# Kernel tuning notes

Hardware: AMD Instinct MI355X
Metric: run time of the kernel (lower is better)

## Reference

```python
import jax, jax.numpy as jnp
import numpy as np

B, S, HID, NH, INTER, VOCAB = 8, 1024, 512, 8, 2048, 30522
EPS = 1e-12


def _layernorm(x, w, b):
    m = jnp.mean(x, axis=-1, keepdims=True)
    v = jnp.mean((x - m) ** 2, axis=-1, keepdims=True)
    return (x - m) * jax.lax.rsqrt(v + EPS) * w + b


def _multihead_mut(x, M):
    # x: (b, s, d); M: (H, s, s). Split d into H heads, mix along the
    # sequence axis per head: out[b,t,h,d] = sum_s x[b,s,h,d] * M[h,s,t]
    b, s, d = x.shape
    xh = x.reshape(b, s, NH, d // NH)
    out = jnp.einsum('bshd,hst->bthd', xh, M)
    return out.reshape(b, s, d)


def setup_inputs() -> dict:
    key = jax.random.key(0)
    ks = jax.random.split(key, 14)
    g = lambda i, shape, scale: jax.random.normal(ks[i], shape, dtype=jnp.float32) * scale
    return {
        'x': jax.random.randint(ks[0], (B, S), 0, VOCAB),
        'word_emb': g(1, (VOCAB, HID), 0.02),
        'pos_emb': g(2, (S, HID), 0.02),
        'tok_emb': g(3, (2, HID), 0.02),
        'emb_ln_w': jnp.ones((HID,), dtype=jnp.float32),
        'emb_ln_b': jnp.zeros((HID,), dtype=jnp.float32),
        'init_d': g(4, (INTER, HID), 0.02),
        'init_b': g(5, (INTER,), 0.02),
        'init_M': g(6, (NH, S, S), 1.0 / np.sqrt(S)),
        'inter0_d': g(7, (INTER, INTER), 1.0 / np.sqrt(INTER)),
        'inter0_b': g(8, (INTER,), 0.02),
        'inter0_M': g(9, (NH, S, S), 1.0 / np.sqrt(S)),
        'final_d': g(10, (HID, INTER), 1.0 / np.sqrt(INTER)),
        'final_b': g(11, (HID,), 0.02),
    }


def reference(x, word_emb, pos_emb, tok_emb, emb_ln_w, emb_ln_b,
              init_d, init_b, init_M, inter0_d, inter0_b, inter0_M,
              final_d, final_b):
    # BertEmbeddings: word + position + token_type(all zeros) -> LayerNorm
    emb = word_emb[x] + pos_emb[None, :, :] + tok_emb[0][None, None, :]
    xo = _layernorm(emb, emb_ln_w, emb_ln_b)  # (B, S, HID)

    # layer 0 (flattened): project to intermediate, per-head seq mix, bias, quad act
    xo = xo @ init_d.T                      # (B, S, INTER)
    xo = _multihead_mut(xo, init_M)
    xo = xo + init_b
    xo = xo * xo                            # activation_quad

    # layer 1 (flattened)
    xo = xo @ inter0_d.T                    # (B, S, INTER)
    xo = _multihead_mut(xo, inter0_M)
    xo = xo + inter0_b
    xo = xo * xo                            # activation_quad

    return xo @ final_d.T + final_b         # (B, S, HID)
```

## Files before the change

kernel.cpp:

```cpp
#include <hip/hip_runtime.h>

typedef _Float16 f16;
typedef _Float16 f16x4 __attribute__((ext_vector_type(4)));
typedef _Float16 f16x8 __attribute__((ext_vector_type(8)));
typedef float    f32x4 __attribute__((ext_vector_type(4)));

#define SEQ   1024
#define HID   512
#define NHEAD 8
#define DH    256
#define INTER 2048
#define BATCH 8
#define ROWS  (BATCH * SEQ)

__device__ __forceinline__ void g2l16(const void* g, void* l) {
  __builtin_amdgcn_global_load_lds(
      (const __attribute__((address_space(1))) void*)g,
      (__attribute__((address_space(3))) void*)l, 16, 0, 0);
}

__device__ __forceinline__ void mm_core(const f16* __restrict__ At,
                                        const f16* __restrict__ Bt,
                                        int K, f32x4 (&acc)[4][4]) {
  __shared__ __align__(16) f16 As[2 * 4096];
  __shared__ __align__(16) f16 Bs[2 * 4096];
  const int tid  = threadIdx.x;
  const int lane = tid & 63, wv = tid >> 6;
  const int wm = (wv >> 1) * 64, wn = (wv & 1) * 64;
  const int lrow  = lane & 15;
  const int kfrag = (lane >> 4) * 8;

  const int c0  = wv * 128 + lane;
  const int r0c = c0 >> 2, q0c = c0 & 3;
  const int c1  = c0 + 64;
  const int r1c = c1 >> 2, q1c = c1 & 3;
  const int ga0 = r0c * K + ((q0c ^ ((r0c >> 1) & 3)) << 3);
  const int ga1 = r1c * K + ((q1c ^ ((r1c >> 1) & 3)) << 3);
  f16* lA0 = &As[wv * 1024];
  f16* lA1 = &As[wv * 1024 + 512];
  f16* lB0 = &Bs[wv * 1024];
  f16* lB1 = &Bs[wv * 1024 + 512];

  int aoff[4], boff[4];
  #pragma unroll
  for (int t = 0; t < 4; ++t) {
    int ra = wm + t * 16 + lrow;
    aoff[t] = ra * 32 + (kfrag ^ (((ra >> 1) & 3) << 3));
    int rb = wn + t * 16 + lrow;
    boff[t] = rb * 32 + (kfrag ^ (((rb >> 1) & 3) << 3));
  }

  g2l16(At + ga0, lA0);
  g2l16(At + ga1, lA1);
  g2l16(Bt + ga0, lB0);
  g2l16(Bt + ga1, lB1);
  __syncthreads();

  int cur = 0;
  for (int k0 = 0; k0 < K; k0 += 32) {
    if (k0 + 32 < K) {
      const int nb = (cur ^ 1) * 4096;
      g2l16(At + (k0 + 32) + ga0, lA0 + nb);
      g2l16(At + (k0 + 32) + ga1, lA1 + nb);
      g2l16(Bt + (k0 + 32) + ga0, lB0 + nb);
      g2l16(Bt + (k0 + 32) + ga1, lB1 + nb);
    }
    const int cb = cur * 4096;
    f16x8 af[4], bf[4];
    #pragma unroll
    for (int t = 0; t < 4; ++t) {
      af[t] = *(const f16x8*)&As[cb + aoff[t]];
      bf[t] = *(const f16x8*)&Bs[cb + boff[t]];
    }
    #pragma unroll
    for (int i = 0; i < 4; ++i)
      #pragma unroll
      for (int j = 0; j < 4; ++j)
        acc[i][j] = __builtin_amdgcn_mfma_f32_16x16x32_f16(af[i], bf[j],
                                                           acc[i][j], 0, 0, 0);
    __syncthreads();
    cur ^= 1;
  }
}

__device__ __forceinline__ void zero_acc(f32x4 (&acc)[4][4]) {
  f32x4 z = {0.f, 0.f, 0.f, 0.f};
  #pragma unroll
  for (int i = 0; i < 4; ++i)
    #pragma unroll
    for (int j = 0; j < 4; ++j) acc[i][j] = z;
}

__global__ __launch_bounds__(256) void gemm_t_kernel(
    const f16* __restrict__ A, const f16* __restrict__ W,
    f16* __restrict__ Xt, int K) {
  int row0 = blockIdx.y * 128, col0 = blockIdx.x * 128;
  f32x4 acc[4][4];
  zero_acc(acc);
  mm_core(A + (size_t)row0 * K, W + (size_t)col0 * K, K, acc);
  int tid = threadIdx.x, lane = tid & 63, wv = tid >> 6;
  int wm = (wv >> 1) * 64, wn = (wv & 1) * 64;
  int cn = lane & 15, rbase = (lane >> 4) * 4;
  int b = row0 >> 10, sbase = row0 & 1023;
  #pragma unroll
  for (int mt = 0; mt < 4; ++mt) {
    int s = sbase + wm + mt * 16 + rbase;
    #pragma unroll
    for (int nt = 0; nt < 4; ++nt) {
      int n = col0 + wn + nt * 16 + cn;
      int h = n >> 8, d = n & 255;
      f16x4 v = {(f16)acc[mt][nt][0], (f16)acc[mt][nt][1],
                 (f16)acc[mt][nt][2], (f16)acc[mt][nt][3]};
      *(f16x4*)&Xt[(((size_t)(b * 8 + h) * 256 + d) << 10) + s] = v;
    }
  }
}

__global__ __launch_bounds__(256) void mut_kernel(
    const f16* __restrict__ Mt, const f16* __restrict__ Xt,
    const float* __restrict__ bias, f16* __restrict__ Y) {
  int b = blockIdx.z >> 3, h = blockIdx.z & 7;
  int t0 = blockIdx.y * 128, d0 = blockIdx.x * 128;
  f32x4 acc[4][4];
  zero_acc(acc);
  const f16* Ap = Mt + ((size_t)h << 20) + ((size_t)t0 << 10);
  const f16* Bp = Xt + (((size_t)(b * 8 + h) * 256 + d0) << 10);
  mm_core(Ap, Bp, SEQ, acc);
  int tid = threadIdx.x, lane = tid & 63, wv = tid >> 6;
  int wm = (wv >> 1) * 64, wn = (wv & 1) * 64;
  int cn = lane & 15, rbase = (lane >> 4) * 4;
  #pragma unroll
  for (int mt = 0; mt < 4; ++mt) {
    int t = t0 + wm + mt * 16 + rbase;
    #pragma unroll
    for (int nt = 0; nt < 4; ++nt) {
      int d = d0 + wn + nt * 16 + cn;
      float bb = bias[(h << 8) + d];
      size_t base = (((size_t)(b << 10) + t) << 11) + (h << 8) + d;
      #pragma unroll
      for (int r = 0; r < 4; ++r) {
        float v = acc[mt][nt][r] + bb;
        Y[base + (size_t)r * INTER] = (f16)(v * v);
      }
    }
  }
}

__global__ __launch_bounds__(256) void gemm_out_kernel(
    const f16* __restrict__ A, const f16* __restrict__ W,
    const float* __restrict__ bias, float* __restrict__ out, int K, int N) {
  int row0 = blockIdx.y * 128, col0 = blockIdx.x * 128;
  f32x4 acc[4][4];
  zero_acc(acc);
  mm_core(A + (size_t)row0 * K, W + (size_t)col0 * K, K, acc);
  int tid = threadIdx.x, lane = tid & 63, wv = tid >> 6;
  int wm = (wv >> 1) * 64, wn = (wv & 1) * 64;
  int cn = lane & 15, rbase = (lane >> 4) * 4;
  #pragma unroll
  for (int mt = 0; mt < 4; ++mt) {
    int r0 = row0 + wm + mt * 16 + rbase;
    #pragma unroll
    for (int nt = 0; nt < 4; ++nt) {
      int col = col0 + wn + nt * 16 + cn;
      float bb = bias[col];
      #pragma unroll
      for (int r = 0; r < 4; ++r)
        out[(size_t)(r0 + r) * N + col] = acc[mt][nt][r] + bb;
    }
  }
}

__global__ __launch_bounds__(256) void embed_ln_kernel(
    const int* __restrict__ x, const float* __restrict__ wemb,
    const float* __restrict__ pemb, const float* __restrict__ temb,
    const float* __restrict__ lnw, const float* __restrict__ lnb,
    f16* __restrict__ out) {
  int row = blockIdx.x;
  int s = row & (SEQ - 1);
  int tok = x[row];
  const float* we = wemb + (size_t)tok * HID;
  const float* pe = pemb + (size_t)s * HID;
  int c = threadIdx.x;
  float e0 = we[c] + pe[c] + temb[c];
  float e1 = we[c + 256] + pe[c + 256] + temb[c + 256];
  float s1 = e0 + e1, s2 = e0 * e0 + e1 * e1;
  #pragma unroll
  for (int off = 32; off > 0; off >>= 1) {
    s1 += __shfl_down(s1, off, 64);
    s2 += __shfl_down(s2, off, 64);
  }
  __shared__ float r1[4], r2[4];
  int wid = threadIdx.x >> 6, lane = threadIdx.x & 63;
  if (lane == 0) { r1[wid] = s1; r2[wid] = s2; }
  __syncthreads();
  float S1 = r1[0] + r1[1] + r1[2] + r1[3];
  float S2 = r2[0] + r2[1] + r2[2] + r2[3];
  float m = S1 * (1.0f / HID);
  float v = S2 * (1.0f / HID) - m * m;
  float inv = rsqrtf(v + 1e-12f);
  f16* o = out + (size_t)row * HID;
  o[c]       = (f16)((e0 - m) * inv * lnw[c]       + lnb[c]);
  o[c + 256] = (f16)((e1 - m) * inv * lnw[c + 256] + lnb[c + 256]);
}

__global__ __launch_bounds__(256) void cast_f16_kernel(
    const float* __restrict__ in, f16* __restrict__ out, int n) {
  int i = (blockIdx.x * 256 + threadIdx.x) * 4;
  if (i < n) {
    float4 v = *(const float4*)(in + i);
    f16x4 o = {(f16)v.x, (f16)v.y, (f16)v.z, (f16)v.w};
    *(f16x4*)(out + i) = o;
  }
}

__global__ __launch_bounds__(256) void mtrans_kernel(
    const float* __restrict__ M, f16* __restrict__ Mt) {
  __shared__ float T[32][33];
  int h = blockIdx.z;
  int s0 = blockIdx.y * 32, t0 = blockIdx.x * 32;
  int tx = threadIdx.x & 31, ty = threadIdx.x >> 5;
  const float* Mh = M + ((size_t)h << 20);
  #pragma unroll
  for (int i = 0; i < 32; i += 8)
    T[ty + i][tx] = Mh[((size_t)(s0 + ty + i) << 10) + t0 + tx];
  __syncthreads();
  f16* Mth = Mt + ((size_t)h << 20);
  #pragma unroll
  for (int i = 0; i < 32; i += 8)
    Mth[((size_t)(t0 + ty + i) << 10) + s0 + tx] = (f16)T[tx][ty + i];
}

extern "C" void kernel_launch(void* const* d_in, const int* in_sizes, int n_in,
                              void* d_out, int out_size, void* d_ws, size_t ws_size,
                              hipStream_t stream) {
  const int*   x        = (const int*)d_in[0];
  const float* wemb     = (const float*)d_in[1];
  const float* pemb     = (const float*)d_in[2];
  const float* temb     = (const float*)d_in[3];
  const float* lnw      = (const float*)d_in[4];
  const float* lnb      = (const float*)d_in[5];
  const float* init_d   = (const float*)d_in[6];
  const float* init_b   = (const float*)d_in[7];
  const float* init_M   = (const float*)d_in[8];
  const float* inter0_d = (const float*)d_in[9];
  const float* inter0_b = (const float*)d_in[10];
  const float* inter0_M = (const float*)d_in[11];
  const float* final_d  = (const float*)d_in[12];
  const float* final_b  = (const float*)d_in[13];
  float* out = (float*)d_out;

  char* ws = (char*)d_ws;
  f16* R0 = (f16*)(ws);
  f16* R1 = (f16*)(ws + 8388608);
  f16* R2 = (f16*)(ws + 10485760);
  f16* R3 = (f16*)(ws + 27262976);
  f16* R4 = (f16*)(ws + 60817408);
  f16* R5 = (f16*)(ws + 94371840);

  embed_ln_kernel<<<ROWS, 256, 0, stream>>>(x, wemb, pemb, temb, lnw, lnb, R0);
  cast_f16_kernel<<<(INTER * HID / 4 + 255) / 256, 256, 0, stream>>>(init_d, R1, INTER * HID);
  mtrans_kernel<<<dim3(32, 32, 8), 256, 0, stream>>>(init_M, R2);
  gemm_t_kernel<<<dim3(INTER / 128, ROWS / 128), 256, 0, stream>>>(R0, R1, R3, HID);
  mut_kernel<<<dim3(DH / 128, SEQ / 128, BATCH * NHEAD), 256, 0, stream>>>(R2, R3, init_b, R4);
  cast_f16_kernel<<<(INTER * INTER / 4 + 255) / 256, 256, 0, stream>>>(inter0_d, R0, INTER * INTER);
  mtrans_kernel<<<dim3(32, 32, 8), 256, 0, stream>>>(inter0_M, R2);
  gemm_t_kernel<<<dim3(INTER / 128, ROWS / 128), 256, 0, stream>>>(R4, R0, R5, INTER);
  mut_kernel<<<dim3(DH / 128, SEQ / 128, BATCH * NHEAD), 256, 0, stream>>>(R2, R5, inter0_b, R3);
  cast_f16_kernel<<<(HID * INTER / 4 + 255) / 256, 256, 0, stream>>>(final_d, R1, HID * INTER);
  gemm_out_kernel<<<dim3(HID / 128, ROWS / 128), 256, 0, stream>>>(R3, R1, final_b, out, INTER, HID);
}
```

Measured before the change: 489.2 us.

## Use 256x256 tiles with triple-buffered LDS pipeline for projection and mix GEMMs

Adds a new GEMM core with 256x256 output tiles, 512 threads, and an 8x4 MFMA accumulator per wave. Global-to-LDS loads are triple-buffered and interleaved with two MFMA half-phases, using explicit waitcnt, barriers and setprio. Both the intermediate projection and the per-head sequence-mix kernels switch to it. The goal is more operand reuse per LDS byte and better latency hiding, at the cost of higher register and LDS pressure and fewer blocks, which can hurt occupancy and wave balance across CUs.

```diff
diff --git a/kernel.cpp b/kernel.cpp
--- a/kernel.cpp
+++ b/kernel.cpp
@@ -17,6 +17,162 @@
   __builtin_amdgcn_global_load_lds(
       (const __attribute__((address_space(1))) void*)g,
       (__attribute__((address_space(3))) void*)l, 16, 0, 0);
+}
+
+__device__ __forceinline__ void mm_core256(const f16* __restrict__ At,
+                                           const f16* __restrict__ Bt,
+                                           int K, f32x4 (&acc)[8][4]) {
+  __shared__ __align__(16) f16 As[3 * 8192];
+  __shared__ __align__(16) f16 Bs[3 * 8192];
+  const int tid  = threadIdx.x;
+  const int lane = tid & 63, wv = tid >> 6;
+  const int wrow = (wv >> 2) * 128, wcol = (wv & 3) * 64;
+
+  const int ch0 = tid, ch1 = tid + 512;
+  const int r0 = ch0 >> 2, s0 = ch0 & 3;
+  const int r1 = ch1 >> 2, s1 = ch1 & 3;
+  const int g0 = r0 * K + ((s0 ^ ((r0 >> 1) & 3)) << 3);
+  const int g1 = r1 * K + ((s1 ^ ((r1 >> 1) & 3)) << 3);
+  const int l0 = wv * 512;
+  const int l1 = 4096 + wv * 512;
+
+  int aoff[8], boff[4];
+  const int q = lane >> 4;
+  #pragma unroll
+  for (int m = 0; m < 8; ++m) {
+    int r = wrow + m * 16 + (lane & 15);
+    aoff[m] = r * 32 + ((q ^ ((r >> 1) & 3)) << 3);
+  }
+  #pragma unroll
+  for (int n = 0; n < 4; ++n) {
+    int r = wcol + n * 16 + (lane & 15);
+    boff[n] = r * 32 + ((q ^ ((r >> 1) & 3)) << 3);
+  }
+
+  const int nt = K >> 5;
+  g2l16(At + g0, &As[l0]);
+  g2l16(At + g1, &As[l1]);
+  g2l16(Bt + g0, &Bs[l0]);
+  g2l16(Bt + g1, &Bs[l1]);
+  g2l16(At + 32 + g0, &As[8192 + l0]);
+  g2l16(At + 32 + g1, &As[8192 + l1]);
+  g2l16(Bt + 32 + g0, &Bs[8192 + l0]);
+  g2l16(Bt + 32 + g1, &Bs[8192 + l1]);
+  __builtin_amdgcn_sched_barrier(0);
+  asm volatile("s_waitcnt vmcnt(4)" ::: "memory");
+  __builtin_amdgcn_s_barrier();
+  __builtin_amdgcn_sched_barrier(0);
+
+  int slot = 0;
+  for (int t = 0; t < nt; ++t) {
+    const int cb = slot * 8192;
+    const int sb = (slot == 0 ? 2 : slot - 1) * 8192;
+    const bool pf = (t + 2 < nt);
+    const int kpre = (t + 2) << 5;
+
+    f16x8 bfr[4], af0[4], af1[4];
+    #pragma unroll
+    for (int n = 0; n < 4; ++n) bfr[n] = *(const f16x8*)&Bs[cb + boff[n]];
+    #pragma unroll
+    for (int m = 0; m < 4; ++m) af0[m] = *(const f16x8*)&As[cb + aoff[m]];
+    if (pf) {
+      g2l16(At + kpre + g0, &As[sb + l0]);
+      g2l16(At + kpre + g1, &As[sb + l1]);
+    }
+    __builtin_amdgcn_s_setprio(1);
+    #pragma unroll
+    for (int m = 0; m < 4; ++m)
+      #pragma unroll
+      for (int n = 0; n < 4; ++n)
+        acc[m][n] = __builtin_amdgcn_mfma_f32_16x16x32_f16(af0[m], bfr[n],
+                                                           acc[m][n], 0, 0, 0);
+    __builtin_amdgcn_s_setprio(0);
+    #pragma unroll
+    for (int m = 0; m < 4; ++m) af1[m] = *(const f16x8*)&As[cb + aoff[m + 4]];
+    if (pf) {
+      g2l16(Bt + kpre + g0, &Bs[sb + l0]);
+      g2l16(Bt + kpre + g1, &Bs[sb + l1]);
+    }
+    __builtin_amdgcn_s_setprio(1);
+    #pragma unroll
+    for (int m = 0; m < 4; ++m)
+      #pragma unroll
+      for (int n = 0; n < 4; ++n)
+        acc[m + 4][n] = __builtin_amdgcn_mfma_f32_16x16x32_f16(af1[m], bfr[n],
+                                                               acc[m + 4][n], 0, 0, 0);
+    __builtin_amdgcn_s_setprio(0);
+    if (t + 1 < nt) {
+      __builtin_amdgcn_sched_barrier(0);
+      if (pf) asm volatile("s_waitcnt vmcnt(4)" ::: "memory");
+      else    asm volatile("s_waitcnt vmcnt(0)" ::: "memory");
+      __builtin_amdgcn_s_barrier();
+      __builtin_amdgcn_sched_barrier(0);
+    }
+    slot = (slot == 2) ? 0 : slot + 1;
+  }
+}
+
+__device__ __forceinline__ void zero_acc8(f32x4 (&acc)[8][4]) {
+  f32x4 z = {0.f, 0.f, 0.f, 0.f};
+  #pragma unroll
+  for (int i = 0; i < 8; ++i)
+    #pragma unroll
+    for (int j = 0; j < 4; ++j) acc[i][j] = z;
+}
+
+__global__ __launch_bounds__(512, 2) void gemm256_t_kernel(
+    const f16* __restrict__ A, const f16* __restrict__ W,
+    f16* __restrict__ Xt, int K) {
+  int row0 = blockIdx.y * 256, col0 = blockIdx.x * 256;
+  f32x4 acc[8][4];
+  zero_acc8(acc);
+  mm_core256(A + (size_t)row0 * K, W + (size_t)col0 * K, K, acc);
+  int tid = threadIdx.x, lane = tid & 63, wv = tid >> 6;
+  int wrow = (wv >> 2) * 128, wcol = (wv & 3) * 64;
+  int cn = lane & 15, rbase = (lane >> 4) * 4;
+  int b = row0 >> 10, sbase = row0 & 1023;
+  #pragma unroll
+  for (int m = 0; m < 8; ++m) {
+    int s = sbase + wrow + m * 16 + rbase;
+    #pragma unroll
+    for (int n = 0; n < 4; ++n) {
+      int col = col0 + wcol + n * 16 + cn;
+      int h = col >> 8, d = col & 255;
+      f16x4 v = {(f16)acc[m][n][0], (f16)acc[m][n][1],
+                 (f16)acc[m][n][2], (f16)acc[m][n][3]};
+      *(f16x4*)&Xt[(((size_t)(b * 8 + h) * 256 + d) << 10) + s] = v;
+    }
+  }
+}
+
+__global__ __launch_bounds__(512, 2) void mut256_kernel(
+    const f16* __restrict__ Mt, const f16* __restrict__ Xt,
+    const float* __restrict__ bias, f16* __restrict__ Y) {
+  int b = blockIdx.z >> 3, h = blockIdx.z & 7;
+  int t0 = blockIdx.y * 256;
+  f32x4 acc[8][4];
+  zero_acc8(acc);
+  const f16* Ap = Mt + ((size_t)h << 20) + ((size_t)t0 << 10);
+  const f16* Bp = Xt + (((size_t)(b * 8 + h)) << 18);
+  mm_core256(Ap, Bp, SEQ, acc);
+  int tid = threadIdx.x, lane = tid & 63, wv = tid >> 6;
+  int wrow = (wv >> 2) * 128, wcol = (wv & 3) * 64;
+  int cn = lane & 15, rbase = (lane >> 4) * 4;
+  #pragma unroll
+  for (int m = 0; m < 8; ++m) {
+    int t = t0 + wrow + m * 16 + rbase;
+    #pragma unroll
+    for (int n = 0; n < 4; ++n) {
+      int d = wcol + n * 16 + cn;
+      float bb = bias[(h << 8) + d];
+      size_t base = (((size_t)(b << 10) + t) << 11) + (h << 8) + d;
+      #pragma unroll
+      for (int r = 0; r < 4; ++r) {
+        float v = acc[m][n][r] + bb;
+        Y[base + (size_t)r * INTER] = (f16)(v * v);
+      }
+    }
+  }
 }
 
 __device__ __forceinline__ void mm_core(const f16* __restrict__ At,
@@ -29,7 +185,6 @@
   const int wm = (wv >> 1) * 64, wn = (wv & 1) * 64;
   const int lrow  = lane & 15;
   const int kfrag = (lane >> 4) * 8;
-
   const int c0  = wv * 128 + lane;
   const int r0c = c0 >> 2, q0c = c0 & 3;
   const int c1  = c0 + 64;
@@ -40,7 +195,6 @@
   f16* lA1 = &As[wv * 1024 + 512];
   f16* lB0 = &Bs[wv * 1024];
   f16* lB1 = &Bs[wv * 1024 + 512];
-
   int aoff[4], boff[4];
   #pragma unroll
   for (int t = 0; t < 4; ++t) {
@@ -49,13 +203,11 @@
     int rb = wn + t * 16 + lrow;
     boff[t] = rb * 32 + (kfrag ^ (((rb >> 1) & 3) << 3));
   }
-
   g2l16(At + ga0, lA0);
   g2l16(At + ga1, lA1);
   g2l16(Bt + ga0, lB0);
   g2l16(Bt + ga1, lB1);
   __syncthreads();
-
   int cur = 0;
   for (int k0 = 0; k0 < K; k0 += 32) {
     if (k0 + 32 < K) {
@@ -89,61 +241,6 @@
   for (int i = 0; i < 4; ++i)
     #pragma unroll
     for (int j = 0; j < 4; ++j) acc[i][j] = z;
-}
-
-__global__ __launch_bounds__(256) void gemm_t_kernel(
-    const f16* __restrict__ A, const f16* __restrict__ W,
-    f16* __restrict__ Xt, int K) {
-  int row0 = blockIdx.y * 128, col0 = blockIdx.x * 128;
-  f32x4 acc[4][4];
-  zero_acc(acc);
-  mm_core(A + (size_t)row0 * K, W + (size_t)col0 * K, K, acc);
-  int tid = threadIdx.x, lane = tid & 63, wv = tid >> 6;
-  int wm = (wv >> 1) * 64, wn = (wv & 1) * 64;
-  int cn = lane & 15, rbase = (lane >> 4) * 4;
-  int b = row0 >> 10, sbase = row0 & 1023;
-  #pragma unroll
-  for (int mt = 0; mt < 4; ++mt) {
-    int s = sbase + wm + mt * 16 + rbase;
-    #pragma unroll
-    for (int nt = 0; nt < 4; ++nt) {
-      int n = col0 + wn + nt * 16 + cn;
-      int h = n >> 8, d = n & 255;
-      f16x4 v = {(f16)acc[mt][nt][0], (f16)acc[mt][nt][1],
-                 (f16)acc[mt][nt][2], (f16)acc[mt][nt][3]};
-      *(f16x4*)&Xt[(((size_t)(b * 8 + h) * 256 + d) << 10) + s] = v;
-    }
-  }
-}
-
-__global__ __launch_bounds__(256) void mut_kernel(
-    const f16* __restrict__ Mt, const f16* __restrict__ Xt,
-    const float* __restrict__ bias, f16* __restrict__ Y) {
-  int b = blockIdx.z >> 3, h = blockIdx.z & 7;
-  int t0 = blockIdx.y * 128, d0 = blockIdx.x * 128;
-  f32x4 acc[4][4];
-  zero_acc(acc);
-  const f16* Ap = Mt + ((size_t)h << 20) + ((size_t)t0 << 10);
-  const f16* Bp = Xt + (((size_t)(b * 8 + h) * 256 + d0) << 10);
-  mm_core(Ap, Bp, SEQ, acc);
-  int tid = threadIdx.x, lane = tid & 63, wv = tid >> 6;
-  int wm = (wv >> 1) * 64, wn = (wv & 1) * 64;
-  int cn = lane & 15, rbase = (lane >> 4) * 4;
-  #pragma unroll
-  for (int mt = 0; mt < 4; ++mt) {
-    int t = t0 + wm + mt * 16 + rbase;
-    #pragma unroll
-    for (int nt = 0; nt < 4; ++nt) {
-      int d = d0 + wn + nt * 16 + cn;
-      float bb = bias[(h << 8) + d];
-      size_t base = (((size_t)(b << 10) + t) << 11) + (h << 8) + d;
-      #pragma unroll
-      for (int r = 0; r < 4; ++r) {
-        float v = acc[mt][nt][r] + bb;
-        Y[base + (size_t)r * INTER] = (f16)(v * v);
-      }
-    }
-  }
 }
 
 __global__ __launch_bounds__(256) void gemm_out_kernel(
@@ -260,12 +357,12 @@
   embed_ln_kernel<<<ROWS, 256, 0, stream>>>(x, wemb, pemb, temb, lnw, lnb, R0);
   cast_f16_kernel<<<(INTER * HID / 4 + 255) / 256, 256, 0, stream>>>(init_d, R1, INTER * HID);
   mtrans_kernel<<<dim3(32, 32, 8), 256, 0, stream>>>(init_M, R2);
-  gemm_t_kernel<<<dim3(INTER / 128, ROWS / 128), 256, 0, stream>>>(R0, R1, R3, HID);
-  mut_kernel<<<dim3(DH / 128, SEQ / 128, BATCH * NHEAD), 256, 0, stream>>>(R2, R3, init_b, R4);
+  gemm256_t_kernel<<<dim3(INTER / 256, ROWS / 256), 512, 0, stream>>>(R0, R1, R3, HID);
+  mut256_kernel<<<dim3(1, SEQ / 256, BATCH * NHEAD), 512, 0, stream>>>(R2, R3, init_b, R4);
   cast_f16_kernel<<<(INTER * INTER / 4 + 255) / 256, 256, 0, stream>>>(inter0_d, R0, INTER * INTER);
   mtrans_kernel<<<dim3(32, 32, 8), 256, 0, stream>>>(inter0_M, R2);
-  gemm_t_kernel<<<dim3(INTER / 128, ROWS / 128), 256, 0, stream>>>(R4, R0, R5, INTER);
-  mut_kernel<<<dim3(DH / 128, SEQ / 128, BATCH * NHEAD), 256, 0, stream>>>(R2, R5, inter0_b, R3);
+  gemm256_t_kernel<<<dim3(INTER / 256, ROWS / 256), 512, 0, stream>>>(R4, R0, R5, INTER);
+  mut256_kernel<<<dim3(1, SEQ / 256, BATCH * NHEAD), 512, 0, stream>>>(R2, R5, inter0_b, R3);
   cast_f16_kernel<<<(HID * INTER / 4 + 255) / 256, 256, 0, stream>>>(final_d, R1, HID * INTER);
   gemm_out_kernel<<<dim3(HID / 128, ROWS / 128), 256, 0, stream>>>(R3, R1, final_b, out, INTER, HID);
 }
```

Result: faster. 425.4 us (-13.0%).

## Use 256x256 block tiles with per-wave private LDS pipelines for projection and mix GEMMs

Applied to the files above, without the earlier changes.

Replaces the 128x128 GEMM core used by the intermediate projection and sequence-mixing kernels with a 256x256 tile. Each wave owns its own LDS region, holding its 128 A rows and 128 B rows, so block-wide __syncthreads is dropped. Prefetch is depth-2 and paced with vmcnt waits, interleaved with MFMA issue. The aim is more arithmetic per LDS/global byte and less barrier overhead. In exchange it needs 64 accumulator tiles per thread with occupancy of 1, and launches fewer blocks (256 per GEMM), which can underfill 256 CUs.

```diff
diff --git a/kernel.cpp b/kernel.cpp
--- a/kernel.cpp
+++ b/kernel.cpp
@@ -17,6 +17,144 @@
   __builtin_amdgcn_global_load_lds(
       (const __attribute__((address_space(1))) void*)g,
       (__attribute__((address_space(3))) void*)l, 16, 0, 0);
+}
+
+__device__ __forceinline__ void mm_core256w(const f16* __restrict__ At,
+                                            const f16* __restrict__ Bt,
+                                            int K, f32x4 (&acc)[8][8]) {
+  __shared__ __align__(16) f16 L[4][2][8192];
+  const int tid  = threadIdx.x;
+  const int lane = tid & 63, wv = tid >> 6;
+  const int wr = (wv >> 1) * 128, wc = (wv & 1) * 128;
+
+  const int srow = lane >> 2, soct = lane & 3;
+  const int swz  = soct ^ ((srow >> 1) & 3);
+  const f16* pA = At + (size_t)(wr + srow) * K + (swz << 3);
+  const f16* pB = Bt + (size_t)(wc + srow) * K + (swz << 3);
+  const size_t sK16 = (size_t)16 * K;
+
+  int aoff[8], boff[8];
+  const int lrow = lane & 15, q = lane >> 4;
+  #pragma unroll
+  for (int m = 0; m < 8; ++m) {
+    int r = m * 16 + lrow;
+    aoff[m] = r * 32 + ((q ^ ((r >> 1) & 3)) << 3);
+    boff[m] = 4096 + aoff[m];
+  }
+
+  f16* const W0 = &L[wv][0][0];
+  f16* const W1 = &L[wv][1][0];
+
+  const int nt = K >> 5;
+  #pragma unroll
+  for (int j = 0; j < 8; ++j) {
+    g2l16(pA + j * sK16,      W0 + j * 512);
+    g2l16(pB + j * sK16,      W0 + 4096 + j * 512);
+  }
+  #pragma unroll
+  for (int j = 0; j < 8; ++j) {
+    g2l16(pA + 32 + j * sK16, W1 + j * 512);
+    g2l16(pB + 32 + j * sK16, W1 + 4096 + j * 512);
+  }
+  asm volatile("s_waitcnt vmcnt(16)" ::: "memory");
+
+  for (int t = 0; t < nt; ++t) {
+    f16* const Wc = (t & 1) ? W1 : W0;
+    const bool pf = (t + 2) < nt;
+    const int kb = (t + 2) << 5;
+
+    f16x8 a[8];
+    #pragma unroll
+    for (int m = 0; m < 8; ++m) a[m] = *(const f16x8*)&Wc[aoff[m]];
+    f16x8 b0 = *(const f16x8*)&Wc[boff[0]];
+
+    #pragma unroll
+    for (int m = 0; m < 8; ++m)
+      acc[m][0] = __builtin_amdgcn_mfma_f32_16x16x32_f16(a[m], b0,
+                                                         acc[m][0], 0, 0, 0);
+    if (pf) {
+      #pragma unroll
+      for (int j = 0; j < 8; ++j) g2l16(pA + kb + j * sK16, Wc + j * 512);
+    }
+    #pragma unroll
+    for (int n = 1; n < 8; ++n) {
+      f16x8 bn = *(const f16x8*)&Wc[boff[n]];
+      #pragma unroll
+      for (int m = 0; m < 8; ++m)
+        acc[m][n] = __builtin_amdgcn_mfma_f32_16x16x32_f16(a[m], bn,
+                                                           acc[m][n], 0, 0, 0);
+    }
+    if (pf) {
+      #pragma unroll
+      for (int j = 0; j < 8; ++j) g2l16(pB + kb + j * sK16, Wc + 4096 + j * 512);
+      asm volatile("s_waitcnt vmcnt(16)" ::: "memory");
+    } else if (t + 1 < nt) {
+      asm volatile("s_waitcnt vmcnt(0)" ::: "memory");
+    }
+  }
+}
+
+__device__ __forceinline__ void zero_acc88(f32x4 (&acc)[8][8]) {
+  f32x4 z = {0.f, 0.f, 0.f, 0.f};
+  #pragma unroll
+  for (int i = 0; i < 8; ++i)
+    #pragma unroll
+    for (int j = 0; j < 8; ++j) acc[i][j] = z;
+}
+
+__global__ __launch_bounds__(256, 1) void gemm256_t_kernel(
+    const f16* __restrict__ A, const f16* __restrict__ W,
+    f16* __restrict__ Xt, int K) {
+  int row0 = blockIdx.y * 256, col0 = blockIdx.x * 256;
+  f32x4 acc[8][8];
+  zero_acc88(acc);
+  mm_core256w(A + (size_t)row0 * K, W + (size_t)col0 * K, K, acc);
+  int tid = threadIdx.x, lane = tid & 63, wv = tid >> 6;
+  int wr = (wv >> 1) * 128, wc = (wv & 1) * 128;
+  int cn = lane & 15, rbase = (lane >> 4) * 4;
+  int b = row0 >> 10, sbase = row0 & 1023;
+  #pragma unroll
+  for (int m = 0; m < 8; ++m) {
+    int s = sbase + wr + m * 16 + rbase;
+    #pragma unroll
+    for (int n = 0; n < 8; ++n) {
+      int col = col0 + wc + n * 16 + cn;
+      int h = col >> 8, d = col & 255;
+      f16x4 v = {(f16)acc[m][n][0], (f16)acc[m][n][1],
+                 (f16)acc[m][n][2], (f16)acc[m][n][3]};
+      *(f16x4*)&Xt[(((size_t)(b * 8 + h) * 256 + d) << 10) + s] = v;
+    }
+  }
+}
+
+__global__ __launch_bounds__(256, 1) void mut256_kernel(
+    const f16* __restrict__ Mt, const f16* __restrict__ Xt,
+    const float* __restrict__ bias, f16* __restrict__ Y) {
+  int b = blockIdx.z >> 3, h = blockIdx.z & 7;
+  int t0 = blockIdx.y * 256;
+  f32x4 acc[8][8];
+  zero_acc88(acc);
+  const f16* Ap = Mt + ((size_t)h << 20) + ((size_t)t0 << 10);
+  const f16* Bp = Xt + (((size_t)(b * 8 + h)) << 18);
+  mm_core256w(Ap, Bp, SEQ, acc);
+  int tid = threadIdx.x, lane = tid & 63, wv = tid >> 6;
+  int wr = (wv >> 1) * 128, wc = (wv & 1) * 128;
+  int cn = lane & 15, rbase = (lane >> 4) * 4;
+  #pragma unroll
+  for (int m = 0; m < 8; ++m) {
+    int t = t0 + wr + m * 16 + rbase;
+    #pragma unroll
+    for (int n = 0; n < 8; ++n) {
+      int d = wc + n * 16 + cn;
+      float bb = bias[(h << 8) + d];
+      size_t base = (((size_t)(b << 10) + t) << 11) + (h << 8) + d;
+      #pragma unroll
+      for (int r = 0; r < 4; ++r) {
+        float v = acc[m][n][r] + bb;
+        Y[base + (size_t)r * INTER] = (f16)(v * v);
+      }
+    }
+  }
 }
 
 __device__ __forceinline__ void mm_core(const f16* __restrict__ At,
@@ -29,7 +167,6 @@
   const int wm = (wv >> 1) * 64, wn = (wv & 1) * 64;
   const int lrow  = lane & 15;
   const int kfrag = (lane >> 4) * 8;
-
   const int c0  = wv * 128 + lane;
   const int r0c = c0 >> 2, q0c = c0 & 3;
   const int c1  = c0 + 64;
@@ -40,7 +177,6 @@
   f16* lA1 = &As[wv * 1024 + 512];
   f16* lB0 = &Bs[wv * 1024];
   f16* lB1 = &Bs[wv * 1024 + 512];
-
   int aoff[4], boff[4];
   #pragma unroll
   for (int t = 0; t < 4; ++t) {
@@ -49,13 +185,11 @@
     int rb = wn + t * 16 + lrow;
     boff[t] = rb * 32 + (kfrag ^ (((rb >> 1) & 3) << 3));
   }
-
   g2l16(At + ga0, lA0);
   g2l16(At + ga1, lA1);
   g2l16(Bt + ga0, lB0);
   g2l16(Bt + ga1, lB1);
   __syncthreads();
-
   int cur = 0;
   for (int k0 = 0; k0 < K; k0 += 32) {
     if (k0 + 32 < K) {
@@ -89,61 +223,6 @@
   for (int i = 0; i < 4; ++i)
     #pragma unroll
     for (int j = 0; j < 4; ++j) acc[i][j] = z;
-}
-
-__global__ __launch_bounds__(256) void gemm_t_kernel(
-    const f16* __restrict__ A, const f16* __restrict__ W,
-    f16* __restrict__ Xt, int K) {
-  int row0 = blockIdx.y * 128, col0 = blockIdx.x * 128;
-  f32x4 acc[4][4];
-  zero_acc(acc);
-  mm_core(A + (size_t)row0 * K, W + (size_t)col0 * K, K, acc);
-  int tid = threadIdx.x, lane = tid & 63, wv = tid >> 6;
-  int wm = (wv >> 1) * 64, wn = (wv & 1) * 64;
-  int cn = lane & 15, rbase = (lane >> 4) * 4;
-  int b = row0 >> 10, sbase = row0 & 1023;
-  #pragma unroll
-  for (int mt = 0; mt < 4; ++mt) {
-    int s = sbase + wm + mt * 16 + rbase;
-    #pragma unroll
-    for (int nt = 0; nt < 4; ++nt) {
-      int n = col0 + wn + nt * 16 + cn;
-      int h = n >> 8, d = n & 255;
-      f16x4 v = {(f16)acc[mt][nt][0], (f16)acc[mt][nt][1],
-                 (f16)acc[mt][nt][2], (f16)acc[mt][nt][3]};
-      *(f16x4*)&Xt[(((size_t)(b * 8 + h) * 256 + d) << 10) + s] = v;
-    }
-  }
-}
-
-__global__ __launch_bounds__(256) void mut_kernel(
-    const f16* __restrict__ Mt, const f16* __restrict__ Xt,
-    const float* __restrict__ bias, f16* __restrict__ Y) {
-  int b = blockIdx.z >> 3, h = blockIdx.z & 7;
-  int t0 = blockIdx.y * 128, d0 = blockIdx.x * 128;
-  f32x4 acc[4][4];
-  zero_acc(acc);
-  const f16* Ap = Mt + ((size_t)h << 20) + ((size_t)t0 << 10);
-  const f16* Bp = Xt + (((size_t)(b * 8 + h) * 256 + d0) << 10);
-  mm_core(Ap, Bp, SEQ, acc);
-  int tid = threadIdx.x, lane = tid & 63, wv = tid >> 6;
-  int wm = (wv >> 1) * 64, wn = (wv & 1) * 64;
-  int cn = lane & 15, rbase = (lane >> 4) * 4;
-  #pragma unroll
-  for (int mt = 0; mt < 4; ++mt) {
-    int t = t0 + wm + mt * 16 + rbase;
-    #pragma unroll
-    for (int nt = 0; nt < 4; ++nt) {
-      int d = d0 + wn + nt * 16 + cn;
-      float bb = bias[(h << 8) + d];
-      size_t base = (((size_t)(b << 10) + t) << 11) + (h << 8) + d;
-      #pragma unroll
-      for (int r = 0; r < 4; ++r) {
-        float v = acc[mt][nt][r] + bb;
-        Y[base + (size_t)r * INTER] = (f16)(v * v);
-      }
-    }
-  }
 }
 
 __global__ __launch_bounds__(256) void gemm_out_kernel(
@@ -260,12 +339,12 @@
   embed_ln_kernel<<<ROWS, 256, 0, stream>>>(x, wemb, pemb, temb, lnw, lnb, R0);
   cast_f16_kernel<<<(INTER * HID / 4 + 255) / 256, 256, 0, stream>>>(init_d, R1, INTER * HID);
   mtrans_kernel<<<dim3(32, 32, 8), 256, 0, stream>>>(init_M, R2);
-  gemm_t_kernel<<<dim3(INTER / 128, ROWS / 128), 256, 0, stream>>>(R0, R1, R3, HID);
-  mut_kernel<<<dim3(DH / 128, SEQ / 128, BATCH * NHEAD), 256, 0, stream>>>(R2, R3, init_b, R4);
+  gemm256_t_kernel<<<dim3(INTER / 256, ROWS / 256), 256, 0, stream>>>(R0, R1, R3, HID);
+  mut256_kernel<<<dim3(1, SEQ / 256, BATCH * NHEAD), 256, 0, stream>>>(R2, R3, init_b, R4);
   cast_f16_kernel<<<(INTER * INTER / 4 + 255) / 256, 256, 0, stream>>>(inter0_d, R0, INTER * INTER);
   mtrans_kernel<<<dim3(32, 32, 8), 256, 0, stream>>>(inter0_M, R2);
-  gemm_t_kernel<<<dim3(INTER / 128, ROWS / 128), 256, 0, stream>>>(R4, R0, R5, INTER);
-  mut_kernel<<<dim3(DH / 128, SEQ / 128, BATCH * NHEAD), 256, 0, stream>>>(R2, R5, inter0_b, R3);
+  gemm256_t_kernel<<<dim3(INTER / 256, ROWS / 256), 256, 0, stream>>>(R4, R0, R5, INTER);
+  mut256_kernel<<<dim3(1, SEQ / 256, BATCH * NHEAD), 256, 0, stream>>>(R2, R5, inter0_b, R3);
   cast_f16_kernel<<<(HID * INTER / 4 + 255) / 256, 256, 0, stream>>>(final_d, R1, HID * INTER);
   gemm_out_kernel<<<dim3(HID / 128, ROWS / 128), 256, 0, stream>>>(R3, R1, final_b, out, INTER, HID);
 }
```

New measurement: 467.9 us. 1.05x faster.
